# Performance work log

Measured on AMD Instinct MI355X. Metric: run time of the kernel, lower is better.

The kernel has to match this reference:

```python
import jax, jax.numpy as jnp
import numpy as np
from jax import lax

# Problem constants (mirroring scalar_born args / init_kwargs)
NY = NX = 400          # interior model size
NS = 4                 # shots
NSRC = 1               # sources per shot
NREC = 100             # receivers per shot
NT = 300               # time steps
CHUNK = 10             # inner scan length (NT % CHUNK == 0)
PML = 20               # pml_width
FD_PAD = 2             # accuracy // 2 for accuracy=4
PAD = PML + FD_PAD
DX = 5.0               # grid_spacing
DT = 5e-4              # dt
PML_FREQ = 25.0
VMAX = 2500.0          # max_vel used for PML profile

# 4th-order central FD coefficients (taps at offsets -2..+2)
C1 = (1.0 / 12, -2.0 / 3, 0.0, 2.0 / 3, -1.0 / 12)        # d/dx, * 1/h
C2 = (-1.0 / 12, 4.0 / 3, -5.0 / 2, 4.0 / 3, -1.0 / 12)   # d2/dx2, * 1/h^2


def _deriv(w, coefs, axis, scale):
    """4th-order central difference along `axis` with zero boundary."""
    pad = [(0, 0)] * w.ndim
    pad[axis] = (2, 2)
    p = jnp.pad(w, pad)
    n = w.shape[axis]
    out = coefs[0] * lax.slice_in_dim(p, 0, n, axis=axis)
    for k in range(1, 5):
        if coefs[k] != 0.0:
            out = out + coefs[k] * lax.slice_in_dim(p, k, k + n, axis=axis)
    return out * scale


def _pml_profiles(n):
    """CPML decay (a) and update (b) 1D profiles over a padded axis."""
    i = jnp.arange(n, dtype=jnp.float32)
    frac = jnp.maximum(jnp.clip((PAD - i) / PML, 0.0, 1.0),
                       jnp.clip((i - (n - 1 - PAD)) / PML, 0.0, 1.0))
    L = PML * DX
    sigma_max = 3.0 * VMAX * np.log(1000.0) / (2.0 * L)
    sigma = sigma_max * frac ** 2
    alpha = np.pi * PML_FREQ
    a = jnp.exp(-(sigma + alpha) * DT)
    b = jnp.where(sigma > 0, sigma / (sigma + alpha) * (a - 1.0), 0.0)
    return a, b


def _propagate(v, scatter, source_amplitudes, source_locations,
               receiver_locations, bg_receiver_locations):
    v_pad = jnp.pad(v, PAD, mode='edge')     # 'replicate' pad for velocity
    sc_pad = jnp.pad(scatter, PAD)           # 'constant' (zero) pad for scatter
    npy, npx = v_pad.shape
    ay, by = _pml_profiles(npy)
    ax, bx = _pml_profiles(npx)
    ay, by = ay[:, None], by[:, None]
    ax, bx = ax[None, :], bx[None, :]
    v2dt2 = (v_pad * DT) ** 2
    born_scale = 2.0 * v_pad * sc_pad * DT * DT  # Born secondary-source scale

    sy = source_locations[..., 0] + PAD          # [ns, nsrc]
    sx = source_locations[..., 1] + PAD
    shot_s = jnp.arange(NS)[:, None]
    v_src = v_pad[sy, sx]
    sc_src = sc_pad[sy, sx]
    # Source scaling as in scalar_born(): bg gets -f*v^2*dt^2,
    # scattered gets -2*f*v*scatter*dt^2 at the source cell.
    f_bg = -source_amplitudes * (v_src ** 2)[..., None] * DT * DT
    f_sc = -2.0 * source_amplitudes * (v_src * sc_src)[..., None] * DT * DT
    f_bg = jnp.moveaxis(f_bg, -1, 0).reshape(NT // CHUNK, CHUNK, NS, NSRC)
    f_sc = jnp.moveaxis(f_sc, -1, 0).reshape(NT // CHUNK, CHUNK, NS, NSRC)

    ry = receiver_locations[..., 0] + PAD
    rx = receiver_locations[..., 1] + PAD
    rby = bg_receiver_locations[..., 0] + PAD
    rbx = bg_receiver_locations[..., 1] + PAD
    shot_r = jnp.arange(NS)[:, None]

    inv_h, inv_h2 = 1.0 / DX, 1.0 / (DX * DX)

    def pml_lap(w, psiy, psix, zetay, zetax):
        # CPML (Pasalic & McGarry) memory variables for 2nd-order scalar wave eq
        dwdy = _deriv(w, C1, -2, inv_h)
        dwdx = _deriv(w, C1, -1, inv_h)
        d2y = _deriv(w, C2, -2, inv_h2)
        d2x = _deriv(w, C2, -1, inv_h2)
        psiy = ay * psiy + by * dwdy
        psix = ax * psix + bx * dwdx
        dpsiy = _deriv(psiy, C1, -2, inv_h)
        dpsix = _deriv(psix, C1, -1, inv_h)
        zetay = ay * zetay + by * (d2y + dpsiy)
        zetax = ax * zetax + bx * (d2x + dpsix)
        lap = d2y + d2x + dpsiy + dpsix + zetay + zetax
        return lap, psiy, psix, zetay, zetax

    def step(carry, fs):
        (wfc, wfp, psiy, psix, zetay, zetax,
         wfcsc, wfpsc, psiysc, psixsc, zetaysc, zetaxsc) = carry
        fb, fsc = fs
        lap, psiy, psix, zetay, zetax = pml_lap(wfc, psiy, psix, zetay, zetax)
        wfn = v2dt2 * lap + 2.0 * wfc - wfp
        wfn = wfn.at[shot_s, sy, sx].add(fb)
        lapsc, psiysc, psixsc, zetaysc, zetaxsc = pml_lap(
            wfcsc, psiysc, psixsc, zetaysc, zetaxsc)
        wfnsc = v2dt2 * lapsc + 2.0 * wfcsc - wfpsc + born_scale * lap
        wfnsc = wfnsc.at[shot_s, sy, sx].add(fsc)
        rec_bg = wfn[shot_r, rby, rbx]
        rec_sc = wfnsc[shot_r, ry, rx]
        new_carry = (wfn, wfc, psiy, psix, zetay, zetax,
                     wfnsc, wfcsc, psiysc, psixsc, zetaysc, zetaxsc)
        return new_carry, (rec_bg, rec_sc)

    chunk = jax.checkpoint(lambda c, xs: lax.scan(step, c, xs))

    z = jnp.zeros((NS, npy, npx), dtype=v.dtype)
    carry0 = (z,) * 12
    carry, (rec_bg, rec_sc) = lax.scan(chunk, carry0, (f_bg, f_sc))
    rec_bg = jnp.moveaxis(rec_bg.reshape(NT, NS, NREC), 0, -1)
    rec_sc = jnp.moveaxis(rec_sc.reshape(NT, NS, NREC), 0, -1)
    return carry, rec_bg, rec_sc


def setup_inputs() -> dict:
    key = jax.random.key(0)
    k = jax.random.split(key, 6)
    v = 1500.0 + 1000.0 * jax.random.uniform(k[0], (NY, NX), jnp.float32)
    scatter = 0.1 * jax.random.normal(k[1], (NY, NX), jnp.float32)
    source_amplitudes = jax.random.normal(k[2], (NS, NSRC, NT), jnp.float32)
    source_locations = jax.random.randint(k[3], (NS, NSRC, 2), 0, NY)
    receiver_locations = jax.random.randint(k[4], (NS, NREC, 2), 0, NY)
    bg_receiver_locations = jax.random.randint(k[5], (NS, NREC, 2), 0, NY)
    return {
        'v': v,
        'scatter': scatter,
        'source_amplitudes': source_amplitudes,
        'source_locations': source_locations,
        'receiver_locations': receiver_locations,
        'bg_receiver_locations': bg_receiver_locations,
    }


def reference(v, scatter, source_amplitudes, source_locations,
              receiver_locations, bg_receiver_locations):
    carry, rec_bg, rec_sc = _propagate(
        v, scatter, source_amplitudes, source_locations,
        receiver_locations, bg_receiver_locations)
    # (final background wavefield, final scattered wavefield,
    #  background receiver amplitudes, scattered receiver amplitudes)
    return (carry[0], carry[6], rec_bg, rec_sc)
```

## Files before the change

### kernel.cpp

```cpp
#include <hip/hip_runtime.h>
#include <hip/hip_bf16.h>


constexpr int NYX  = 400;
constexpr int NS   = 4;
constexpr int NREC = 100;
constexpr int NT   = 300;
constexpr int PAD  = 22;
constexpr int NP   = 444;
constexpr int NP2  = NP * NP;
constexpr int SNP2 = NS * NP2;
constexpr float DT    = 0.0005f;
constexpr float INVH  = 0.2f;
constexpr float INVH2 = 0.04f;
constexpr float C1A = 1.0f / 12.0f;
constexpr float C1B = 2.0f / 3.0f;
constexpr float C2A = -1.0f / 12.0f;
constexpr float C2B = 4.0f / 3.0f;
constexpr float C2C = -2.5f;

__device__ __align__(16) float g_w[2][2 * SNP2];
__device__ __align__(16) float g_px[2][2 * SNP2];
__device__ __align__(16) float g_py[2][2 * SNP2];
__device__ __align__(16) float g_zx[2 * SNP2];
__device__ __align__(16) float g_zy[2 * SNP2];
__device__ __align__(16) float g_vb[2 * NP2];
__device__ float g_pa[NP];
__device__ float g_pb[NP];
__device__ float g_fbg[NT * NS];
__device__ float g_fsc[NT * NS];
__device__ int   g_spos[2 * NS];
__device__ int   g_mode;

__device__ __forceinline__ int clampi(int v, int lo, int hi) {
    return v < lo ? lo : (v > hi ? hi : v);
}
__device__ __forceinline__ float in_ld(const void* p, int i) {
    if (g_mode) return __bfloat162float(((const __hip_bfloat16*)p)[i]);
    return ((const float*)p)[i];
}
__device__ __forceinline__ void out_st(void* p, int i, float v) {
    if (g_mode) ((__hip_bfloat16*)p)[i] = __float2bfloat16(v);
    else        ((float*)p)[i] = v;
}
__device__ __forceinline__ float4 ld4(const float* w, int s, int yy, int ip) {
    if ((unsigned)yy >= (unsigned)NP) return make_float4(0.f, 0.f, 0.f, 0.f);
    return *(const float4*)(w + 2 * (s * NP2 + yy * NP + 2 * ip));
}
__device__ __forceinline__ float4 shup4(float4 v) {
    return make_float4(__shfl_up(v.x, 1), __shfl_up(v.y, 1),
                       __shfl_up(v.z, 1), __shfl_up(v.w, 1));
}
__device__ __forceinline__ float4 shdn4(float4 v) {
    return make_float4(__shfl_down(v.x, 1), __shfl_down(v.y, 1),
                       __shfl_down(v.z, 1), __shfl_down(v.w, 1));
}

__global__ void detect_mode(const void* vptr) {
    if (threadIdx.x == 0 && blockIdx.x == 0) {
        const __hip_bfloat16* p = (const __hip_bfloat16*)vptr;
        int ok = 1;
        for (int i = 0; i < 32; i += 2) {
            float f = __bfloat162float(p[i]);
            if (!(f >= 1000.f && f <= 3000.f)) ok = 0;
        }
        g_mode = ok;
    }
}

__global__ void zero_state() {
    int i = blockIdx.x * blockDim.x + threadIdx.x;
    if (i >= SNP2 / 2) return;
    float4 z = make_float4(0.f, 0.f, 0.f, 0.f);
    ((float4*)g_w[0])[i] = z;  ((float4*)g_w[1])[i] = z;
    ((float4*)g_px[0])[i] = z; ((float4*)g_px[1])[i] = z;
    ((float4*)g_py[0])[i] = z; ((float4*)g_py[1])[i] = z;
    ((float4*)g_zx)[i] = z;    ((float4*)g_zy)[i] = z;
}

__global__ void prep_pad(const void* __restrict__ v, const void* __restrict__ sc) {
    int i = blockIdx.x * blockDim.x + threadIdx.x;
    if (i >= NP2) return;
    int y = i / NP, x = i % NP;
    int vy = clampi(y - PAD, 0, NYX - 1);
    int vx = clampi(x - PAD, 0, NYX - 1);
    float vv = in_ld(v, vy * NYX + vx);
    float vd = vv * DT;
    float s = 0.f;
    if (y >= PAD && y < PAD + NYX && x >= PAD && x < PAD + NYX)
        s = in_ld(sc, (y - PAD) * NYX + (x - PAD));
    g_vb[2 * i]     = vd * vd;
    g_vb[2 * i + 1] = 2.f * vv * s * DT * DT;
    if (i < NP) {
        float fi = (float)i;
        float f1 = fminf(fmaxf((22.f - fi) * 0.05f, 0.f), 1.f);
        float f2 = fminf(fmaxf((fi - 421.f) * 0.05f, 0.f), 1.f);
        float frac = fmaxf(f1, f2);
        float sigma = 259.0408229f * frac * frac;
        const float alpha = 78.53981634f;
        float a = expf(-(sigma + alpha) * DT);
        g_pa[i] = a;
        g_pb[i] = (sigma > 0.f) ? sigma / (sigma + alpha) * (a - 1.f) : 0.f;
    }
}

__global__ void prep_src(const void* __restrict__ amp, const int* __restrict__ sloc,
                         const void* __restrict__ v, const void* __restrict__ sc) {
    int i = blockIdx.x * blockDim.x + threadIdx.x;
    if (i >= NT * NS) return;
    int s = i % NS, t = i / NS;
    int ly = clampi(sloc[s * 2 + 0], 0, NYX - 1);
    int lx = clampi(sloc[s * 2 + 1], 0, NYX - 1);
    float a  = in_ld(amp, s * NT + t);
    float vv = in_ld(v,  ly * NYX + lx);
    float ss = in_ld(sc, ly * NYX + lx);
    g_fbg[i] = -a * vv * vv * DT * DT;
    g_fsc[i] = -2.f * a * vv * ss * DT * DT;
    if (i < NS) {
        g_spos[2 * i]     = ly + PAD;
        g_spos[2 * i + 1] = lx + PAD;
    }
}

__global__ void __launch_bounds__(256, 7)
step_fused(int t, const int* __restrict__ rloc, const int* __restrict__ rbloc,
           void* __restrict__ out) {
    const int i = threadIdx.x;
    const int bid = blockIdx.x;
    const int s = (bid >> 1) & 3;
    const int k = bid >> 3;
    const int y = ((bid & 1) ? 222 : 0) + (35 * k) % 222;
    const int cur = t & 1, nxt = cur ^ 1;

    if (t > 0 && y == 0 && i < 2 * NREC) {
        int r = i % NREC;
        bool isbg = i < NREC;
        const int* rl = isbg ? rbloc : rloc;
        int ry = clampi(rl[(s * NREC + r) * 2 + 0], 0, NYX - 1) + PAD;
        int rx = clampi(rl[(s * NREC + r) * 2 + 1], 0, NYX - 1) + PAD;
        float val = g_w[cur][2 * (s * NP2 + ry * NP + rx) + (isbg ? 0 : 1)];
        int base = isbg ? (2 * SNP2) : (2 * SNP2 + NS * NREC * NT);
        out_st(out, base + (s * NREC + r) * NT + (t - 1), val);
    }

    const int wid  = i >> 6;
    const int lane = i & 63;
    const int ip   = 60 * wid + lane - 2;
    const bool inb   = (unsigned)ip < 222u;
    const bool owner = (lane >= 2) && (lane < 62) && inb;

    const int x0 = 2 * ip, x1 = x0 + 1;
    const int yx  = y * NP + x0;
    const int idx = s * NP2 + yx;

    float4 w4 = make_float4(0.f, 0.f, 0.f, 0.f);
    if (inb) w4 = *(const float4*)(g_w[cur] + 2 * idx);

    float4 wl = shup4(w4);
    float4 wr = shdn4(w4);

    const bool pxreg = (ip <= 11 || ip >= 210);
    float pbx0 = 0.f, pbx1 = 0.f, pax0 = 0.f, pax1 = 0.f;
    float d2x_b0 = 0.f, d2x_b1 = 0.f, d2x_s0 = 0.f, d2x_s1 = 0.f;
    float4 pxn = make_float4(0.f, 0.f, 0.f, 0.f);
    if (inb) {
        d2x_b0 = (C2A * (wl.x + wr.x) + C2B * (wl.z + w4.z) + C2C * w4.x) * INVH2;
        d2x_s0 = (C2A * (wl.y + wr.y) + C2B * (wl.w + w4.w) + C2C * w4.y) * INVH2;
        d2x_b1 = (C2A * (wl.z + wr.z) + C2B * (w4.x + wr.x) + C2C * w4.z) * INVH2;
        d2x_s1 = (C2A * (wl.w + wr.w) + C2B * (w4.y + wr.y) + C2C * w4.w) * INVH2;
        pbx0 = g_pb[x0]; pbx1 = g_pb[x1];
        pax0 = g_pa[x0]; pax1 = g_pa[x1];
        if (pxreg && pbx0 != 0.f) {
            float4 pxo = *(const float4*)(g_px[cur] + 2 * idx);
            float dwb0 = (C1A * wl.x - C1B * wl.z + C1B * w4.z - C1A * wr.x) * INVH;
            float dws0 = (C1A * wl.y - C1B * wl.w + C1B * w4.w - C1A * wr.y) * INVH;
            float dwb1 = (C1A * wl.z - C1B * w4.x + C1B * wr.x - C1A * wr.z) * INVH;
            float dws1 = (C1A * wl.w - C1B * w4.y + C1B * wr.y - C1A * wr.w) * INVH;
            pxn.x = pax0 * pxo.x + pbx0 * dwb0;
            pxn.y = pax0 * pxo.y + pbx0 * dws0;
            pxn.z = pax1 * pxo.z + pbx1 * dwb1;
            pxn.w = pax1 * pxo.w + pbx1 * dws1;
            if (owner)
                *(float4*)(g_px[nxt] + 2 * idx) = pxn;
        }
    }

    float dpx_b0 = 0.f, dpx_b1 = 0.f, dpx_s0 = 0.f, dpx_s1 = 0.f;
    {
        float4 pl = shup4(pxn);
        float4 pr = shdn4(pxn);
        if (pxreg) {
            dpx_b0 = (C1A * pl.x - C1B * pl.z + C1B * pxn.z - C1A * pr.x) * INVH;
            dpx_s0 = (C1A * pl.y - C1B * pl.w + C1B * pxn.w - C1A * pr.y) * INVH;
            dpx_b1 = (C1A * pl.z - C1B * pxn.x + C1B * pr.x - C1A * pr.z) * INVH;
            dpx_s1 = (C1A * pl.w - C1B * pxn.y + C1B * pr.y - C1A * pr.w) * INVH;
        }
    }

    if (!owner) return;

    const float pby = g_pb[y];
    const bool yframe = (y <= 23 || y >= 420);
    float d2y_b0, d2y_b1, d2y_s0, d2y_s1;
    float dpy_b0 = 0.f, dpy_b1 = 0.f, dpy_s0 = 0.f, dpy_s1 = 0.f;
    if (yframe) {
        float4 wy[9];
        #pragma unroll
        for (int kk = 0; kk < 9; ++kk)
            wy[kk] = (kk == 4) ? w4 : ld4(g_w[cur], s, y - 4 + kk, ip);
        d2y_b0 = (C2A * (wy[2].x + wy[6].x) + C2B * (wy[3].x + wy[5].x) + C2C * wy[4].x) * INVH2;
        d2y_s0 = (C2A * (wy[2].y + wy[6].y) + C2B * (wy[3].y + wy[5].y) + C2C * wy[4].y) * INVH2;
        d2y_b1 = (C2A * (wy[2].z + wy[6].z) + C2B * (wy[3].z + wy[5].z) + C2C * wy[4].z) * INVH2;
        d2y_s1 = (C2A * (wy[2].w + wy[6].w) + C2B * (wy[3].w + wy[5].w) + C2C * wy[4].w) * INVH2;
        float4 pn[5];
        #pragma unroll
        for (int kk = 0; kk < 5; ++kk) {
            int yy = y - 2 + kk;
            float pbv = ((unsigned)yy < (unsigned)NP) ? g_pb[yy] : 0.f;
            float4 r = make_float4(0.f, 0.f, 0.f, 0.f);
            if (pbv != 0.f) {
                float pav = g_pa[yy];
                float4 po = *(const float4*)(g_py[cur] + 2 * (s * NP2 + yy * NP + x0));
                float db0 = (C1A * wy[kk].x - C1B * wy[kk+1].x + C1B * wy[kk+3].x - C1A * wy[kk+4].x) * INVH;
                float ds0 = (C1A * wy[kk].y - C1B * wy[kk+1].y + C1B * wy[kk+3].y - C1A * wy[kk+4].y) * INVH;
                float db1 = (C1A * wy[kk].z - C1B * wy[kk+1].z + C1B * wy[kk+3].z - C1A * wy[kk+4].z) * INVH;
                float ds1 = (C1A * wy[kk].w - C1B * wy[kk+1].w + C1B * wy[kk+3].w - C1A * wy[kk+4].w) * INVH;
                r.x = pav * po.x + pbv * db0;  r.y = pav * po.y + pbv * ds0;
                r.z = pav * po.z + pbv * db1;  r.w = pav * po.w + pbv * ds1;
            }
            pn[kk] = r;
        }
        dpy_b0 = (C1A * pn[0].x - C1B * pn[1].x + C1B * pn[3].x - C1A * pn[4].x) * INVH;
        dpy_s0 = (C1A * pn[0].y - C1B * pn[1].y + C1B * pn[3].y - C1A * pn[4].y) * INVH;
        dpy_b1 = (C1A * pn[0].z - C1B * pn[1].z + C1B * pn[3].z - C1A * pn[4].z) * INVH;
        dpy_s1 = (C1A * pn[0].w - C1B * pn[1].w + C1B * pn[3].w - C1A * pn[4].w) * INVH;
        if (pby != 0.f)
            *(float4*)(g_py[nxt] + 2 * idx) = pn[2];
    } else {
        float4 m2 = *(const float4*)(g_w[cur] + 2 * (idx - 2 * NP));
        float4 m1 = *(const float4*)(g_w[cur] + 2 * (idx - NP));
        float4 p1 = *(const float4*)(g_w[cur] + 2 * (idx + NP));
        float4 p2 = *(const float4*)(g_w[cur] + 2 * (idx + 2 * NP));
        d2y_b0 = (C2A * (m2.x + p2.x) + C2B * (m1.x + p1.x) + C2C * w4.x) * INVH2;
        d2y_s0 = (C2A * (m2.y + p2.y) + C2B * (m1.y + p1.y) + C2C * w4.y) * INVH2;
        d2y_b1 = (C2A * (m2.z + p2.z) + C2B * (m1.z + p1.z) + C2C * w4.z) * INVH2;
        d2y_s1 = (C2A * (m2.w + p2.w) + C2B * (m1.w + p1.w) + C2C * w4.w) * INVH2;
    }

    float zy_b0 = 0.f, zy_b1 = 0.f, zy_s0 = 0.f, zy_s1 = 0.f;
    float zx_b0 = 0.f, zx_b1 = 0.f, zx_s0 = 0.f, zx_s1 = 0.f;
    if (pby != 0.f) {
        float pay = g_pa[y];
        float4 zo = *(const float4*)(g_zy + 2 * idx);
        zy_b0 = pay * zo.x + pby * (d2y_b0 + dpy_b0);
        zy_s0 = pay * zo.y + pby * (d2y_s0 + dpy_s0);
        zy_b1 = pay * zo.z + pby * (d2y_b1 + dpy_b1);
        zy_s1 = pay * zo.w + pby * (d2y_s1 + dpy_s1);
        *(float4*)(g_zy + 2 * idx) = make_float4(zy_b0, zy_s0, zy_b1, zy_s1);
    }
    if (pbx0 != 0.f) {
        float4 zo = *(const float4*)(g_zx + 2 * idx);
        zx_b0 = pax0 * zo.x + pbx0 * (d2x_b0 + dpx_b0);
        zx_s0 = pax0 * zo.y + pbx0 * (d2x_s0 + dpx_s0);
        zx_b1 = pax1 * zo.z + pbx1 * (d2x_b1 + dpx_b1);
        zx_s1 = pax1 * zo.w + pbx1 * (d2x_s1 + dpx_s1);
        *(float4*)(g_zx + 2 * idx) = make_float4(zx_b0, zx_s0, zx_b1, zx_s1);
    }

    float4 vb   = *(const float4*)(g_vb + 2 * yx);
    float4 prev = *(const float4*)(g_w[nxt] + 2 * idx);
    float lap_b0 = d2y_b0 + d2x_b0 + dpy_b0 + dpx_b0 + zy_b0 + zx_b0;
    float lap_s0 = d2y_s0 + d2x_s0 + dpy_s0 + dpx_s0 + zy_s0 + zx_s0;
    float lap_b1 = d2y_b1 + d2x_b1 + dpy_b1 + dpx_b1 + zy_b1 + zx_b1;
    float lap_s1 = d2y_s1 + d2x_s1 + dpy_s1 + dpx_s1 + zy_s1 + zx_s1;
    float wn_b0 = vb.x * lap_b0 + 2.f * w4.x - prev.x;
    float wn_s0 = vb.x * lap_s0 + 2.f * w4.y - prev.y + vb.y * lap_b0;
    float wn_b1 = vb.z * lap_b1 + 2.f * w4.z - prev.z;
    float wn_s1 = vb.z * lap_s1 + 2.f * w4.w - prev.w + vb.w * lap_b1;
    if (y == g_spos[2 * s]) {
        int sx = g_spos[2 * s + 1];
        if (sx == x0)      { wn_b0 += g_fbg[t * NS + s]; wn_s0 += g_fsc[t * NS + s]; }
        else if (sx == x1) { wn_b1 += g_fbg[t * NS + s]; wn_s1 += g_fsc[t * NS + s]; }
    }
    *(float4*)(g_w[nxt] + 2 * idx) = make_float4(wn_b0, wn_s0, wn_b1, wn_s1);
}

__global__ void finalize(const int* __restrict__ rloc, const int* __restrict__ rbloc,
                         void* __restrict__ out) {
    int i = blockIdx.x * blockDim.x + threadIdx.x;
    const float* w0 = g_w[0];
    if (i < SNP2) {
        out_st(out, i,        w0[2 * i]);
        out_st(out, SNP2 + i, w0[2 * i + 1]);
    }
    if (i < 2 * NS * NREC) {
        bool isbg = i < NS * NREC;
        int k = isbg ? i : i - NS * NREC;
        int s = k / NREC, r = k % NREC;
        const int* rl = isbg ? rbloc : rloc;
        int ry = clampi(rl[(s * NREC + r) * 2 + 0], 0, NYX - 1) + PAD;
        int rx = clampi(rl[(s * NREC + r) * 2 + 1], 0, NYX - 1) + PAD;
        float val = w0[2 * (s * NP2 + ry * NP + rx) + (isbg ? 0 : 1)];
        int base = isbg ? (2 * SNP2) : (2 * SNP2 + NS * NREC * NT);
        out_st(out, base + (s * NREC + r) * NT + (NT - 1), val);
    }
}

extern "C" void kernel_launch(void* const* d_in, const int* in_sizes, int n_in,
                              void* d_out, int out_size, void* d_ws, size_t ws_size,
                              hipStream_t stream) {
    const void* v   = d_in[0];
    const void* sc  = d_in[1];
    const void* amp = d_in[2];
    const int* sloc  = (const int*)d_in[3];
    const int* rloc  = (const int*)d_in[4];
    const int* rbloc = (const int*)d_in[5];

    detect_mode<<<1, 64, 0, stream>>>(v);
    zero_state<<<(SNP2 / 2 + 255) / 256, 256, 0, stream>>>();
    prep_pad<<<(NP2 + 255) / 256, 256, 0, stream>>>(v, sc);
    prep_src<<<(NT * NS + 255) / 256, 256, 0, stream>>>(amp, sloc, v, sc);

    for (int t = 0; t < NT; ++t)
        step_fused<<<NS * NP, 256, 0, stream>>>(t, rloc, rbloc, d_out);

    finalize<<<(SNP2 + 255) / 256, 256, 0, stream>>>(rloc, rbloc, d_out);
}
```

Baseline: 2.429 ms.

## Replace wavefront shuffles with direct neighbour loads and one-thread-per-pair row mapping

Each block now maps one thread to each of the 222 column pairs in a row. The old layout used four overlapping 60-wide wavefront windows with halo lanes. Left and right neighbour values now come from direct float4 loads, which the cache should serve, instead of cross-lane shuffles, and the x-PML psi values of neighbours are recomputed per thread. This removes the redundant halo lanes and the shuffle instructions, and it also changes the block-to-row assignment from a strided permutation to sequential rows. The cost is extra global/L1 loads and duplicated psi computation in the PML columns.

```diff
diff --git a/kernel.cpp b/kernel.cpp
--- a/kernel.cpp
+++ b/kernel.cpp
@@ -47,13 +47,26 @@
     if ((unsigned)yy >= (unsigned)NP) return make_float4(0.f, 0.f, 0.f, 0.f);
     return *(const float4*)(w + 2 * (s * NP2 + yy * NP + 2 * ip));
 }
-__device__ __forceinline__ float4 shup4(float4 v) {
-    return make_float4(__shfl_up(v.x, 1), __shfl_up(v.y, 1),
-                       __shfl_up(v.z, 1), __shfl_up(v.w, 1));
-}
-__device__ __forceinline__ float4 shdn4(float4 v) {
-    return make_float4(__shfl_down(v.x, 1), __shfl_down(v.y, 1),
-                       __shfl_down(v.z, 1), __shfl_down(v.w, 1));
+__device__ __forceinline__ float4 psix_new(int p, float4 wm, float4 wc, float4 wp,
+                                           const float* pxc, int base) {
+    float4 r = make_float4(0.f, 0.f, 0.f, 0.f);
+    if ((unsigned)p < 222u) {
+        float pb0 = g_pb[2 * p];
+        if (pb0 != 0.f) {
+            float pb1 = g_pb[2 * p + 1];
+            float pa0 = g_pa[2 * p], pa1 = g_pa[2 * p + 1];
+            float4 pxo = *(const float4*)(pxc + 2 * (base + 2 * p));
+            float dwb0 = (C1A * wm.x - C1B * wm.z + C1B * wc.z - C1A * wp.x) * INVH;
+            float dws0 = (C1A * wm.y - C1B * wm.w + C1B * wc.w - C1A * wp.y) * INVH;
+            float dwb1 = (C1A * wm.z - C1B * wc.x + C1B * wp.x - C1A * wp.z) * INVH;
+            float dws1 = (C1A * wm.w - C1B * wc.y + C1B * wp.y - C1A * wp.w) * INVH;
+            r.x = pa0 * pxo.x + pb0 * dwb0;
+            r.y = pa0 * pxo.y + pb0 * dws0;
+            r.z = pa1 * pxo.z + pb1 * dwb1;
+            r.w = pa1 * pxo.w + pb1 * dws1;
+        }
+    }
+    return r;
 }
 
 __global__ void detect_mode(const void* vptr) {
@@ -128,8 +141,7 @@
     const int i = threadIdx.x;
     const int bid = blockIdx.x;
     const int s = (bid >> 1) & 3;
-    const int k = bid >> 3;
-    const int y = ((bid & 1) ? 222 : 0) + (35 * k) % 222;
+    const int y = ((bid & 1) ? 222 : 0) + (bid >> 3);
     const int cur = t & 1, nxt = cur ^ 1;
 
     if (t > 0 && y == 0 && i < 2 * NREC) {
@@ -143,61 +155,45 @@
         out_st(out, base + (s * NREC + r) * NT + (t - 1), val);
     }
 
-    const int wid  = i >> 6;
-    const int lane = i & 63;
-    const int ip   = 60 * wid + lane - 2;
-    const bool inb   = (unsigned)ip < 222u;
-    const bool owner = (lane >= 2) && (lane < 62) && inb;
+    const int ip = i;
+    if (ip >= 222) return;
 
     const int x0 = 2 * ip, x1 = x0 + 1;
-    const int yx  = y * NP + x0;
-    const int idx = s * NP2 + yx;
-
-    float4 w4 = make_float4(0.f, 0.f, 0.f, 0.f);
-    if (inb) w4 = *(const float4*)(g_w[cur] + 2 * idx);
-
-    float4 wl = shup4(w4);
-    float4 wr = shdn4(w4);
+    const int yx   = y * NP + x0;
+    const int idx  = s * NP2 + yx;
+    const int base = s * NP2 + y * NP;
+    const float4 z4 = make_float4(0.f, 0.f, 0.f, 0.f);
+    const float* wc = g_w[cur];
+
+    float4 w4  = *(const float4*)(wc + 2 * idx);
+    float4 wl4 = (ip >= 1)   ? *(const float4*)(wc + 2 * idx - 4) : z4;
+    float4 wr4 = (ip <= 220) ? *(const float4*)(wc + 2 * idx + 4) : z4;
+
+    float d2x_b0 = (C2A * (wl4.x + wr4.x) + C2B * (wl4.z + w4.z) + C2C * w4.x) * INVH2;
+    float d2x_s0 = (C2A * (wl4.y + wr4.y) + C2B * (wl4.w + w4.w) + C2C * w4.y) * INVH2;
+    float d2x_b1 = (C2A * (wl4.z + wr4.z) + C2B * (w4.x + wr4.x) + C2C * w4.z) * INVH2;
+    float d2x_s1 = (C2A * (wl4.w + wr4.w) + C2B * (w4.y + wr4.y) + C2C * w4.w) * INVH2;
+
+    const float pbx0 = g_pb[x0], pbx1 = g_pb[x1];
+    const float pax0 = g_pa[x0], pax1 = g_pa[x1];
 
     const bool pxreg = (ip <= 11 || ip >= 210);
-    float pbx0 = 0.f, pbx1 = 0.f, pax0 = 0.f, pax1 = 0.f;
-    float d2x_b0 = 0.f, d2x_b1 = 0.f, d2x_s0 = 0.f, d2x_s1 = 0.f;
-    float4 pxn = make_float4(0.f, 0.f, 0.f, 0.f);
-    if (inb) {
-        d2x_b0 = (C2A * (wl.x + wr.x) + C2B * (wl.z + w4.z) + C2C * w4.x) * INVH2;
-        d2x_s0 = (C2A * (wl.y + wr.y) + C2B * (wl.w + w4.w) + C2C * w4.y) * INVH2;
-        d2x_b1 = (C2A * (wl.z + wr.z) + C2B * (w4.x + wr.x) + C2C * w4.z) * INVH2;
-        d2x_s1 = (C2A * (wl.w + wr.w) + C2B * (w4.y + wr.y) + C2C * w4.w) * INVH2;
-        pbx0 = g_pb[x0]; pbx1 = g_pb[x1];
-        pax0 = g_pa[x0]; pax1 = g_pa[x1];
-        if (pxreg && pbx0 != 0.f) {
-            float4 pxo = *(const float4*)(g_px[cur] + 2 * idx);
-            float dwb0 = (C1A * wl.x - C1B * wl.z + C1B * w4.z - C1A * wr.x) * INVH;
-            float dws0 = (C1A * wl.y - C1B * wl.w + C1B * w4.w - C1A * wr.y) * INVH;
-            float dwb1 = (C1A * wl.z - C1B * w4.x + C1B * wr.x - C1A * wr.z) * INVH;
-            float dws1 = (C1A * wl.w - C1B * w4.y + C1B * wr.y - C1A * wr.w) * INVH;
-            pxn.x = pax0 * pxo.x + pbx0 * dwb0;
-            pxn.y = pax0 * pxo.y + pbx0 * dws0;
-            pxn.z = pax1 * pxo.z + pbx1 * dwb1;
-            pxn.w = pax1 * pxo.w + pbx1 * dws1;
-            if (owner)
-                *(float4*)(g_px[nxt] + 2 * idx) = pxn;
-        }
-    }
-
+    float4 pxn = z4;
     float dpx_b0 = 0.f, dpx_b1 = 0.f, dpx_s0 = 0.f, dpx_s1 = 0.f;
-    {
-        float4 pl = shup4(pxn);
-        float4 pr = shdn4(pxn);
-        if (pxreg) {
-            dpx_b0 = (C1A * pl.x - C1B * pl.z + C1B * pxn.z - C1A * pr.x) * INVH;
-            dpx_s0 = (C1A * pl.y - C1B * pl.w + C1B * pxn.w - C1A * pr.y) * INVH;
-            dpx_b1 = (C1A * pl.z - C1B * pxn.x + C1B * pr.x - C1A * pr.z) * INVH;
-            dpx_s1 = (C1A * pl.w - C1B * pxn.y + C1B * pr.y - C1A * pr.w) * INVH;
-        }
-    }
-
-    if (!owner) return;
+    if (pxreg) {
+        float4 wll = (ip >= 2)   ? *(const float4*)(wc + 2 * idx - 8) : z4;
+        float4 wrr = (ip <= 219) ? *(const float4*)(wc + 2 * idx + 8) : z4;
+        const float* pxc = g_px[cur];
+        float4 pxn_l = psix_new(ip - 1, wll, wl4, w4, pxc, base);
+        pxn          = psix_new(ip,     wl4, w4, wr4, pxc, base);
+        float4 pxn_r = psix_new(ip + 1, w4, wr4, wrr, pxc, base);
+        dpx_b0 = (C1A * pxn_l.x - C1B * pxn_l.z + C1B * pxn.z - C1A * pxn_r.x) * INVH;
+        dpx_s0 = (C1A * pxn_l.y - C1B * pxn_l.w + C1B * pxn.w - C1A * pxn_r.y) * INVH;
+        dpx_b1 = (C1A * pxn_l.z - C1B * pxn.x + C1B * pxn_r.x - C1A * pxn_r.z) * INVH;
+        dpx_s1 = (C1A * pxn_l.w - C1B * pxn.y + C1B * pxn_r.y - C1A * pxn_r.w) * INVH;
+        if (pbx0 != 0.f)
+            *(float4*)(g_px[nxt] + 2 * idx) = pxn;
+    }
 
     const float pby = g_pb[y];
     const bool yframe = (y <= 23 || y >= 420);
@@ -207,7 +203,7 @@
         float4 wy[9];
         #pragma unroll
         for (int kk = 0; kk < 9; ++kk)
-            wy[kk] = (kk == 4) ? w4 : ld4(g_w[cur], s, y - 4 + kk, ip);
+            wy[kk] = (kk == 4) ? w4 : ld4(wc, s, y - 4 + kk, ip);
         d2y_b0 = (C2A * (wy[2].x + wy[6].x) + C2B * (wy[3].x + wy[5].x) + C2C * wy[4].x) * INVH2;
         d2y_s0 = (C2A * (wy[2].y + wy[6].y) + C2B * (wy[3].y + wy[5].y) + C2C * wy[4].y) * INVH2;
         d2y_b1 = (C2A * (wy[2].z + wy[6].z) + C2B * (wy[3].z + wy[5].z) + C2C * wy[4].z) * INVH2;
@@ -217,7 +213,7 @@
         for (int kk = 0; kk < 5; ++kk) {
             int yy = y - 2 + kk;
             float pbv = ((unsigned)yy < (unsigned)NP) ? g_pb[yy] : 0.f;
-            float4 r = make_float4(0.f, 0.f, 0.f, 0.f);
+            float4 r = z4;
             if (pbv != 0.f) {
                 float pav = g_pa[yy];
                 float4 po = *(const float4*)(g_py[cur] + 2 * (s * NP2 + yy * NP + x0));
@@ -237,10 +233,10 @@
         if (pby != 0.f)
             *(float4*)(g_py[nxt] + 2 * idx) = pn[2];
     } else {
-        float4 m2 = *(const float4*)(g_w[cur] + 2 * (idx - 2 * NP));
-        float4 m1 = *(const float4*)(g_w[cur] + 2 * (idx - NP));
-        float4 p1 = *(const float4*)(g_w[cur] + 2 * (idx + NP));
-        float4 p2 = *(const float4*)(g_w[cur] + 2 * (idx + 2 * NP));
+        float4 m2 = *(const float4*)(wc + 2 * (idx - 2 * NP));
+        float4 m1 = *(const float4*)(wc + 2 * (idx - NP));
+        float4 p1 = *(const float4*)(wc + 2 * (idx + NP));
+        float4 p2 = *(const float4*)(wc + 2 * (idx + 2 * NP));
         d2y_b0 = (C2A * (m2.x + p2.x) + C2B * (m1.x + p1.x) + C2C * w4.x) * INVH2;
         d2y_s0 = (C2A * (m2.y + p2.y) + C2B * (m1.y + p1.y) + C2C * w4.y) * INVH2;
         d2y_b1 = (C2A * (m2.z + p2.z) + C2B * (m1.z + p1.z) + C2C * w4.z) * INVH2;
```

Measured after the change: 3.560 ms. +46.6%, slower.

## Process two interior rows per block and split frame rows into dedicated blocks

Applied to the files above, without the earlier changes.

Blocks that cover the interior now each handle two adjacent rows and load six rows of the wavefield once, so the vertical stencil loads are shared between the two output rows. The PML frame rows (y<24 and y>=420) get their own blocks that keep the full CPML path. The block-to-row mapping is rearranged so each group of 8 consecutive block IDs covers all shot/half pairs, giving 984 blocks instead of 1776. Launch bounds drop to 5 waves because of the extra register pressure, which lowers occupancy. Fewer blocks also means less launch and tail overhead per step.

```diff
diff --git a/kernel.cpp b/kernel.cpp
--- a/kernel.cpp
+++ b/kernel.cpp
@@ -10,6 +10,7 @@
 constexpr int NP   = 444;
 constexpr int NP2  = NP * NP;
 constexpr int SNP2 = NS * NP2;
+constexpr int NBLK = 984;
 constexpr float DT    = 0.0005f;
 constexpr float INVH  = 0.2f;
 constexpr float INVH2 = 0.04f;
@@ -122,54 +123,27 @@
     }
 }
 
-__global__ void __launch_bounds__(256, 7)
-step_fused(int t, const int* __restrict__ rloc, const int* __restrict__ rbloc,
-           void* __restrict__ out) {
-    const int i = threadIdx.x;
-    const int bid = blockIdx.x;
-    const int s = (bid >> 1) & 3;
-    const int k = bid >> 3;
-    const int y = ((bid & 1) ? 222 : 0) + (35 * k) % 222;
-    const int cur = t & 1, nxt = cur ^ 1;
-
-    if (t > 0 && y == 0 && i < 2 * NREC) {
-        int r = i % NREC;
-        bool isbg = i < NREC;
-        const int* rl = isbg ? rbloc : rloc;
-        int ry = clampi(rl[(s * NREC + r) * 2 + 0], 0, NYX - 1) + PAD;
-        int rx = clampi(rl[(s * NREC + r) * 2 + 1], 0, NYX - 1) + PAD;
-        float val = g_w[cur][2 * (s * NP2 + ry * NP + rx) + (isbg ? 0 : 1)];
-        int base = isbg ? (2 * SNP2) : (2 * SNP2 + NS * NREC * NT);
-        out_st(out, base + (s * NREC + r) * NT + (t - 1), val);
-    }
-
-    const int wid  = i >> 6;
-    const int lane = i & 63;
-    const int ip   = 60 * wid + lane - 2;
-    const bool inb   = (unsigned)ip < 222u;
-    const bool owner = (lane >= 2) && (lane < 62) && inb;
-
+__device__ __forceinline__ void row_interior(
+    int t, int s, int y, int ip, bool inb, bool owner, bool pxreg,
+    float pbx0, float pbx1, float pax0, float pax1,
+    float4 ym2, float4 ym1, float4 w4, float4 yp1, float4 yp2,
+    int cur, int nxt)
+{
     const int x0 = 2 * ip, x1 = x0 + 1;
     const int yx  = y * NP + x0;
     const int idx = s * NP2 + yx;
-
-    float4 w4 = make_float4(0.f, 0.f, 0.f, 0.f);
-    if (inb) w4 = *(const float4*)(g_w[cur] + 2 * idx);
+    const float4 z4 = make_float4(0.f, 0.f, 0.f, 0.f);
 
     float4 wl = shup4(w4);
     float4 wr = shdn4(w4);
 
-    const bool pxreg = (ip <= 11 || ip >= 210);
-    float pbx0 = 0.f, pbx1 = 0.f, pax0 = 0.f, pax1 = 0.f;
-    float d2x_b0 = 0.f, d2x_b1 = 0.f, d2x_s0 = 0.f, d2x_s1 = 0.f;
-    float4 pxn = make_float4(0.f, 0.f, 0.f, 0.f);
+    float d2x_b0 = 0.f, d2x_s0 = 0.f, d2x_b1 = 0.f, d2x_s1 = 0.f;
+    float4 pxn = z4;
     if (inb) {
         d2x_b0 = (C2A * (wl.x + wr.x) + C2B * (wl.z + w4.z) + C2C * w4.x) * INVH2;
         d2x_s0 = (C2A * (wl.y + wr.y) + C2B * (wl.w + w4.w) + C2C * w4.y) * INVH2;
         d2x_b1 = (C2A * (wl.z + wr.z) + C2B * (w4.x + wr.x) + C2C * w4.z) * INVH2;
         d2x_s1 = (C2A * (wl.w + wr.w) + C2B * (w4.y + wr.y) + C2C * w4.w) * INVH2;
-        pbx0 = g_pb[x0]; pbx1 = g_pb[x1];
-        pax0 = g_pa[x0]; pax1 = g_pa[x1];
         if (pxreg && pbx0 != 0.f) {
             float4 pxo = *(const float4*)(g_px[cur] + 2 * idx);
             float dwb0 = (C1A * wl.x - C1B * wl.z + C1B * w4.z - C1A * wr.x) * INVH;
@@ -185,6 +159,144 @@
         }
     }
 
+    float dpx_b0 = 0.f, dpx_s0 = 0.f, dpx_b1 = 0.f, dpx_s1 = 0.f;
+    {
+        float4 pl = shup4(pxn);
+        float4 pr = shdn4(pxn);
+        if (pxreg) {
+            dpx_b0 = (C1A * pl.x - C1B * pl.z + C1B * pxn.z - C1A * pr.x) * INVH;
+            dpx_s0 = (C1A * pl.y - C1B * pl.w + C1B * pxn.w - C1A * pr.y) * INVH;
+            dpx_b1 = (C1A * pl.z - C1B * pxn.x + C1B * pr.x - C1A * pr.z) * INVH;
+            dpx_s1 = (C1A * pl.w - C1B * pxn.y + C1B * pr.y - C1A * pr.w) * INVH;
+        }
+    }
+    if (!owner) return;
+
+    float d2y_b0 = (C2A * (ym2.x + yp2.x) + C2B * (ym1.x + yp1.x) + C2C * w4.x) * INVH2;
+    float d2y_s0 = (C2A * (ym2.y + yp2.y) + C2B * (ym1.y + yp1.y) + C2C * w4.y) * INVH2;
+    float d2y_b1 = (C2A * (ym2.z + yp2.z) + C2B * (ym1.z + yp1.z) + C2C * w4.z) * INVH2;
+    float d2y_s1 = (C2A * (ym2.w + yp2.w) + C2B * (ym1.w + yp1.w) + C2C * w4.w) * INVH2;
+
+    float zx_b0 = 0.f, zx_s0 = 0.f, zx_b1 = 0.f, zx_s1 = 0.f;
+    if (pbx0 != 0.f) {
+        float4 zo = *(const float4*)(g_zx + 2 * idx);
+        zx_b0 = pax0 * zo.x + pbx0 * (d2x_b0 + dpx_b0);
+        zx_s0 = pax0 * zo.y + pbx0 * (d2x_s0 + dpx_s0);
+        zx_b1 = pax1 * zo.z + pbx1 * (d2x_b1 + dpx_b1);
+        zx_s1 = pax1 * zo.w + pbx1 * (d2x_s1 + dpx_s1);
+        *(float4*)(g_zx + 2 * idx) = make_float4(zx_b0, zx_s0, zx_b1, zx_s1);
+    }
+
+    float4 vb   = *(const float4*)(g_vb + 2 * yx);
+    float4 prev = *(const float4*)(g_w[nxt] + 2 * idx);
+    float lap_b0 = d2y_b0 + d2x_b0 + dpx_b0 + zx_b0;
+    float lap_s0 = d2y_s0 + d2x_s0 + dpx_s0 + zx_s0;
+    float lap_b1 = d2y_b1 + d2x_b1 + dpx_b1 + zx_b1;
+    float lap_s1 = d2y_s1 + d2x_s1 + dpx_s1 + zx_s1;
+    float wn_b0 = vb.x * lap_b0 + 2.f * w4.x - prev.x;
+    float wn_s0 = vb.x * lap_s0 + 2.f * w4.y - prev.y + vb.y * lap_b0;
+    float wn_b1 = vb.z * lap_b1 + 2.f * w4.z - prev.z;
+    float wn_s1 = vb.z * lap_s1 + 2.f * w4.w - prev.w + vb.w * lap_b1;
+    if (y == g_spos[2 * s]) {
+        int sx = g_spos[2 * s + 1];
+        if (sx == x0)      { wn_b0 += g_fbg[t * NS + s]; wn_s0 += g_fsc[t * NS + s]; }
+        else if (sx == x1) { wn_b1 += g_fbg[t * NS + s]; wn_s1 += g_fsc[t * NS + s]; }
+    }
+    *(float4*)(g_w[nxt] + 2 * idx) = make_float4(wn_b0, wn_s0, wn_b1, wn_s1);
+}
+
+__global__ void __launch_bounds__(256, 5)
+step_fused(int t, const int* __restrict__ rloc, const int* __restrict__ rbloc,
+           void* __restrict__ out) {
+    const int i = threadIdx.x;
+    const int bid = blockIdx.x;
+    const int xcd = bid & 7;
+    const int s = xcd >> 1;
+    const int half = xcd & 1;
+    const int k = bid >> 3;
+    const int cur = t & 1, nxt = cur ^ 1;
+    const bool isframe = (k < 24);
+    const int y0 = isframe ? (half ? 420 + k : k)
+                           : ((half ? 222 : 24) + 2 * (k - 24));
+
+    if (t > 0 && isframe && y0 == 0 && i < 2 * NREC) {
+        int r = i % NREC;
+        bool isbg = i < NREC;
+        const int* rl = isbg ? rbloc : rloc;
+        int ry = clampi(rl[(s * NREC + r) * 2 + 0], 0, NYX - 1) + PAD;
+        int rx = clampi(rl[(s * NREC + r) * 2 + 1], 0, NYX - 1) + PAD;
+        float val = g_w[cur][2 * (s * NP2 + ry * NP + rx) + (isbg ? 0 : 1)];
+        int base = isbg ? (2 * SNP2) : (2 * SNP2 + NS * NREC * NT);
+        out_st(out, base + (s * NREC + r) * NT + (t - 1), val);
+    }
+
+    const int wid  = i >> 6;
+    const int lane = i & 63;
+    const int ip   = 60 * wid + lane - 2;
+    const bool inb   = (unsigned)ip < 222u;
+    const bool owner = (lane >= 2) && (lane < 62) && inb;
+
+    const int x0 = 2 * ip, x1 = x0 + 1;
+    const float4 z4 = make_float4(0.f, 0.f, 0.f, 0.f);
+    const float* wc = g_w[cur];
+
+    float pbx0 = 0.f, pbx1 = 0.f, pax0 = 0.f, pax1 = 0.f;
+    if (inb) {
+        pbx0 = g_pb[x0]; pbx1 = g_pb[x1];
+        pax0 = g_pa[x0]; pax1 = g_pa[x1];
+    }
+    const bool pxreg = (ip <= 11 || ip >= 210);
+
+    if (!isframe) {
+        const int idx0 = s * NP2 + y0 * NP + x0;
+        float4 wm2 = z4, wm1 = z4, wa = z4, wb = z4, wp1 = z4, wp2 = z4;
+        if (inb) {
+            wm2 = *(const float4*)(wc + 2 * (idx0 - 2 * NP));
+            wm1 = *(const float4*)(wc + 2 * (idx0 - NP));
+            wa  = *(const float4*)(wc + 2 * idx0);
+            wb  = *(const float4*)(wc + 2 * (idx0 + NP));
+            wp1 = *(const float4*)(wc + 2 * (idx0 + 2 * NP));
+            wp2 = *(const float4*)(wc + 2 * (idx0 + 3 * NP));
+        }
+        row_interior(t, s, y0,     ip, inb, owner, pxreg, pbx0, pbx1, pax0, pax1,
+                     wm2, wm1, wa, wb, wp1, cur, nxt);
+        row_interior(t, s, y0 + 1, ip, inb, owner, pxreg, pbx0, pbx1, pax0, pax1,
+                     wm1, wa, wb, wp1, wp2, cur, nxt);
+        return;
+    }
+
+    const int y = y0;
+    const int yx  = y * NP + x0;
+    const int idx = s * NP2 + yx;
+
+    float4 w4 = z4;
+    if (inb) w4 = *(const float4*)(wc + 2 * idx);
+
+    float4 wl = shup4(w4);
+    float4 wr = shdn4(w4);
+
+    float d2x_b0 = 0.f, d2x_b1 = 0.f, d2x_s0 = 0.f, d2x_s1 = 0.f;
+    float4 pxn = z4;
+    if (inb) {
+        d2x_b0 = (C2A * (wl.x + wr.x) + C2B * (wl.z + w4.z) + C2C * w4.x) * INVH2;
+        d2x_s0 = (C2A * (wl.y + wr.y) + C2B * (wl.w + w4.w) + C2C * w4.y) * INVH2;
+        d2x_b1 = (C2A * (wl.z + wr.z) + C2B * (w4.x + wr.x) + C2C * w4.z) * INVH2;
+        d2x_s1 = (C2A * (wl.w + wr.w) + C2B * (w4.y + wr.y) + C2C * w4.w) * INVH2;
+        if (pxreg && pbx0 != 0.f) {
+            float4 pxo = *(const float4*)(g_px[cur] + 2 * idx);
+            float dwb0 = (C1A * wl.x - C1B * wl.z + C1B * w4.z - C1A * wr.x) * INVH;
+            float dws0 = (C1A * wl.y - C1B * wl.w + C1B * w4.w - C1A * wr.y) * INVH;
+            float dwb1 = (C1A * wl.z - C1B * w4.x + C1B * wr.x - C1A * wr.z) * INVH;
+            float dws1 = (C1A * wl.w - C1B * w4.y + C1B * wr.y - C1A * wr.w) * INVH;
+            pxn.x = pax0 * pxo.x + pbx0 * dwb0;
+            pxn.y = pax0 * pxo.y + pbx0 * dws0;
+            pxn.z = pax1 * pxo.z + pbx1 * dwb1;
+            pxn.w = pax1 * pxo.w + pbx1 * dws1;
+            if (owner)
+                *(float4*)(g_px[nxt] + 2 * idx) = pxn;
+        }
+    }
+
     float dpx_b0 = 0.f, dpx_b1 = 0.f, dpx_s0 = 0.f, dpx_s1 = 0.f;
     {
         float4 pl = shup4(pxn);
@@ -196,18 +308,16 @@
             dpx_s1 = (C1A * pl.w - C1B * pxn.y + C1B * pr.y - C1A * pr.w) * INVH;
         }
     }
-
     if (!owner) return;
 
     const float pby = g_pb[y];
-    const bool yframe = (y <= 23 || y >= 420);
     float d2y_b0, d2y_b1, d2y_s0, d2y_s1;
     float dpy_b0 = 0.f, dpy_b1 = 0.f, dpy_s0 = 0.f, dpy_s1 = 0.f;
-    if (yframe) {
+    {
         float4 wy[9];
         #pragma unroll
         for (int kk = 0; kk < 9; ++kk)
-            wy[kk] = (kk == 4) ? w4 : ld4(g_w[cur], s, y - 4 + kk, ip);
+            wy[kk] = (kk == 4) ? w4 : ld4(wc, s, y - 4 + kk, ip);
         d2y_b0 = (C2A * (wy[2].x + wy[6].x) + C2B * (wy[3].x + wy[5].x) + C2C * wy[4].x) * INVH2;
         d2y_s0 = (C2A * (wy[2].y + wy[6].y) + C2B * (wy[3].y + wy[5].y) + C2C * wy[4].y) * INVH2;
         d2y_b1 = (C2A * (wy[2].z + wy[6].z) + C2B * (wy[3].z + wy[5].z) + C2C * wy[4].z) * INVH2;
@@ -217,7 +327,7 @@
         for (int kk = 0; kk < 5; ++kk) {
             int yy = y - 2 + kk;
             float pbv = ((unsigned)yy < (unsigned)NP) ? g_pb[yy] : 0.f;
-            float4 r = make_float4(0.f, 0.f, 0.f, 0.f);
+            float4 r = z4;
             if (pbv != 0.f) {
                 float pav = g_pa[yy];
                 float4 po = *(const float4*)(g_py[cur] + 2 * (s * NP2 + yy * NP + x0));
@@ -236,15 +346,6 @@
         dpy_s1 = (C1A * pn[0].w - C1B * pn[1].w + C1B * pn[3].w - C1A * pn[4].w) * INVH;
         if (pby != 0.f)
             *(float4*)(g_py[nxt] + 2 * idx) = pn[2];
-    } else {
-        float4 m2 = *(const float4*)(g_w[cur] + 2 * (idx - 2 * NP));
-        float4 m1 = *(const float4*)(g_w[cur] + 2 * (idx - NP));
-        float4 p1 = *(const float4*)(g_w[cur] + 2 * (idx + NP));
-        float4 p2 = *(const float4*)(g_w[cur] + 2 * (idx + 2 * NP));
-        d2y_b0 = (C2A * (m2.x + p2.x) + C2B * (m1.x + p1.x) + C2C * w4.x) * INVH2;
-        d2y_s0 = (C2A * (m2.y + p2.y) + C2B * (m1.y + p1.y) + C2C * w4.y) * INVH2;
-        d2y_b1 = (C2A * (m2.z + p2.z) + C2B * (m1.z + p1.z) + C2C * w4.z) * INVH2;
-        d2y_s1 = (C2A * (m2.w + p2.w) + C2B * (m1.w + p1.w) + C2C * w4.w) * INVH2;
     }
 
     float zy_b0 = 0.f, zy_b1 = 0.f, zy_s0 = 0.f, zy_s1 = 0.f;
@@ -322,7 +423,7 @@
     prep_src<<<(NT * NS + 255) / 256, 256, 0, stream>>>(amp, sloc, v, sc);
 
     for (int t = 0; t < NT; ++t)
-        step_fused<<<NS * NP, 256, 0, stream>>>(t, rloc, rbloc, d_out);
+        step_fused<<<NBLK, 256, 0, stream>>>(t, rloc, rbloc, d_out);
 
     finalize<<<(SNP2 + 255) / 256, 256, 0, stream>>>(rloc, rbloc, d_out);
 }
```

Result: faster. 2.116 ms (-12.9%).
